# Performance work log

Hardware: AMD Instinct MI355X
Metric: run time of the kernel (lower is better)

The kernel has to match this reference:

```python
import jax, jax.numpy as jnp
import numpy as np

EPS = 1e-05


def setup_inputs() -> dict:
    key = jax.random.key(0)
    kx, kw, kb, kg, kp, kq = jax.random.split(key, 6)
    B, S, D = 32, 1024, 1024
    x = jax.random.normal(kx, (B, S, D), dtype=jnp.float32)
    # Linear(input_size, input_size) params
    W = jax.random.normal(kw, (D, D), dtype=jnp.float32) / np.sqrt(D)
    b = jax.random.normal(kb, (D,), dtype=jnp.float32) * 0.01
    gold_opinion = jax.random.uniform(kg, (B, S, 5), dtype=jnp.float32)
    predict_opinion = jax.random.uniform(kp, (B, S, 5), dtype=jnp.float32)
    gold_prob = jax.random.uniform(kq, (), dtype=jnp.float32)
    return {"x": x, "W": W, "b": b, "gold_opinion": gold_opinion,
            "predict_opinion": predict_opinion, "gold_prob": gold_prob}


def reference(x, W, b, gold_opinion, predict_opinion, gold_prob):
    # x: [B, S, D]
    S = x.shape[-2]
    x_tran = jnp.einsum('bsd,ed->bse', x, W) + b           # Linear: x @ W^T + b
    weights = jnp.einsum('bsd,btd->bst', x_tran, x)        # QK^T -> [B, S, S]

    idx = jnp.arange(S)
    location = jnp.abs(idx[None, :] - idx[:, None]).astype(x.dtype)  # [S, S]
    weights = weights * (1.0 / (location + EPS))           # distance decay

    # use_opinion = True branch
    gold_op = gold_opinion[:, :, 1] + gold_opinion[:, :, 2]          # [B, S]
    pred_op = predict_opinion[:, :, 3] + predict_opinion[:, :, 4]    # [B, S]
    opinion_weights = gold_prob * gold_op + (1.0 - gold_prob) * pred_op
    weights = weights * opinion_weights[:, :, None]

    weights = jnp.exp(jnp.tanh(weights))                   # pseudo-softmax numerator
    off_diag = (location != 0).astype(weights.dtype)       # eye(S) == 0 mask
    weights = weights * off_diag
    weights = weights / (jnp.sum(weights, axis=-1, keepdims=True) + EPS)
    return jnp.einsum('bst,btd->bsd', weights, x)
```

## Files before the change

kernel.cpp:

```cpp
#include <hip/hip_runtime.h>

#define EPSF 1e-5f

typedef _Float16 f16x8 __attribute__((ext_vector_type(8)));
typedef float f32x4 __attribute__((ext_vector_type(4)));

__device__ __forceinline__ void gload_lds16(const _Float16* g, _Float16* l) {
  __builtin_amdgcn_global_load_lds(
      (const __attribute__((address_space(1))) unsigned int*)g,
      (__attribute__((address_space(3))) unsigned int*)l, 16, 0, 0);
}

__device__ __forceinline__ f16x8 cvt8(float4 a, float4 b) {
  f16x8 h;
  h[0] = (_Float16)a.x; h[1] = (_Float16)a.y; h[2] = (_Float16)a.z; h[3] = (_Float16)a.w;
  h[4] = (_Float16)b.x; h[5] = (_Float16)b.y; h[6] = (_Float16)b.z; h[7] = (_Float16)b.w;
  return h;
}

__device__ __forceinline__ float frcp(float x) {
  float r;
  asm("v_rcp_f32 %0, %1" : "=v"(r) : "v"(x));
  return r;
}

__device__ __forceinline__ void gemm256_run(const _Float16* __restrict__ Ag,
                                            const _Float16* __restrict__ Bg,
                                            _Float16* lds, f32x4 (&acc)[8][4]) {
  const int tid = threadIdx.x;
  const int wave = tid >> 6, lane = tid & 63;
  const int wm = wave >> 2, wn = wave & 3;
  const int quad = lane >> 4, nl = lane & 15;
  const int swz = nl & 7;
  const long stg_off = (long)(wave * 8 + (lane >> 3)) * 1024 +
                       (((lane & 7) ^ (lane >> 3)) * 8);

#pragma unroll
  for (int i = 0; i < 8; ++i)
#pragma unroll
    for (int j = 0; j < 4; ++j) acc[i][j] = (f32x4){0.f, 0.f, 0.f, 0.f};

  f16x8 af[4], bf[4];

#define STG(G, T1, q, isB)                                                   \
  gload_lds16((G) + (long)(q) * 65536 + stg_off + (T1) * 64,                 \
              lds + (((T1) & 1) * 32768 + (isB) * 16384 + (q) * 4096 + wave * 512))
#define LDB4(bb, ksub)                                                       \
  {                                                                          \
    const _Float16* pB_ = lds + (bb) * 32768 + 16384 + (wn * 64 + nl) * 64 + \
                          ((((ksub) * 4 + quad) ^ swz) * 8);                 \
    _Pragma("unroll") for (int j_ = 0; j_ < 4; ++j_)                         \
        bf[j_] = *(const f16x8*)(pB_ + j_ * 1024);                           \
  }
#define LDA4(bb, mq, ksub)                                                   \
  {                                                                          \
    const _Float16* pA_ = lds + (bb) * 32768 +                               \
                          (wm * 128 + (mq) * 64 + nl) * 64 +                 \
                          ((((ksub) * 4 + quad) ^ swz) * 8);                 \
    _Pragma("unroll") for (int i_ = 0; i_ < 4; ++i_)                         \
        af[i_] = *(const f16x8*)(pA_ + i_ * 1024);                           \
  }
#define MFMA16(mq)                                                           \
  {                                                                          \
    __builtin_amdgcn_s_setprio(1);                                           \
    _Pragma("unroll") for (int i_ = 0; i_ < 4; ++i_)                         \
        _Pragma("unroll") for (int j_ = 0; j_ < 4; ++j_)                     \
            acc[(mq) * 4 + i_][j_] = __builtin_amdgcn_mfma_f32_16x16x32_f16( \
                af[i_], bf[j_], acc[(mq) * 4 + i_][j_], 0, 0, 0);            \
    __builtin_amdgcn_s_setprio(0);                                           \
  }
#define BAR __builtin_amdgcn_s_barrier()
#define SCHED0 __builtin_amdgcn_sched_barrier(0)
#define LGKM0 asm volatile("s_waitcnt lgkmcnt(0)" ::: "memory")
#define VMW2 asm volatile("s_waitcnt vmcnt(2)" ::: "memory")
#define VMW0 asm volatile("s_waitcnt vmcnt(0)" ::: "memory")

  STG(Bg, 0, 0, 1); STG(Bg, 0, 1, 1);
  STG(Ag, 0, 0, 0); STG(Ag, 0, 2, 0);
  STG(Bg, 0, 2, 1); STG(Bg, 0, 3, 1);
  STG(Ag, 0, 1, 0); STG(Ag, 0, 3, 0);
  VMW2;
  BAR;

#pragma unroll 2
  for (int T = 0; T < 15; ++T) {
    const int bb = T & 1;
    LDB4(bb, 0); LDA4(bb, 0, 0);
    STG(Bg, T + 1, 0, 1); STG(Bg, T + 1, 1, 1);
    SCHED0; BAR; LGKM0; SCHED0; MFMA16(0); VMW2; BAR;
    LDA4(bb, 1, 0);
    STG(Ag, T + 1, 0, 0); STG(Ag, T + 1, 2, 0);
    SCHED0; BAR; LGKM0; SCHED0; MFMA16(1); BAR;
    LDB4(bb, 1); LDA4(bb, 0, 1);
    STG(Bg, T + 1, 2, 1); STG(Bg, T + 1, 3, 1);
    SCHED0; BAR; LGKM0; SCHED0; MFMA16(0); BAR;
    LDA4(bb, 1, 1);
    STG(Ag, T + 1, 1, 0); STG(Ag, T + 1, 3, 0);
    SCHED0; BAR; LGKM0; SCHED0; MFMA16(1); VMW2; BAR;
  }
  {
    LDB4(1, 0); LDA4(1, 0, 0);
    SCHED0; BAR; LGKM0; SCHED0; MFMA16(0); VMW0; BAR;
    LDA4(1, 1, 0);
    SCHED0; BAR; LGKM0; SCHED0; MFMA16(1); BAR;
    LDB4(1, 1); LDA4(1, 0, 1);
    SCHED0; BAR; LGKM0; SCHED0; MFMA16(0); BAR;
    LDA4(1, 1, 1);
    SCHED0; BAR; LGKM0; SCHED0; MFMA16(1); BAR;
  }
#undef VMW0
#undef VMW2
#undef LGKM0
#undef SCHED0
#undef BAR
#undef MFMA16
#undef LDA4
#undef LDB4
#undef STG
}

__global__ void prep_opin_k(const float* __restrict__ gold, const float* __restrict__ pred,
                            const float* __restrict__ gprob, float* __restrict__ opin, int n) {
  int i = blockIdx.x * 256 + threadIdx.x;
  if (i >= n) return;
  float gp = gprob[0];
  float go = gold[i * 5 + 1] + gold[i * 5 + 2];
  float po = pred[i * 5 + 3] + pred[i * 5 + 4];
  opin[i] = gp * go + (1.0f - gp) * po;
}

__global__ __launch_bounds__(256) void prep_h_k(const float* __restrict__ src,
                                                _Float16* __restrict__ dst) {
  long i = ((long)blockIdx.x * 256 + threadIdx.x) * 8;
  float4 a = *(const float4*)(src + i);
  float4 b = *(const float4*)(src + i + 4);
  *(f16x8*)(dst + i) = cvt8(a, b);
}

__global__ __launch_bounds__(256) void prep_x_k(const float* __restrict__ x,
                                                _Float16* __restrict__ Xh,
                                                _Float16* __restrict__ XhT) {
  __shared__ _Float16 T[64][66];
  const int d0 = blockIdx.x * 64, t0 = blockIdx.y * 64;
  const long base = (long)blockIdx.z * 1024;
  const int c = threadIdx.x & 63, tr = threadIdx.x >> 6;
#pragma unroll
  for (int k = 0; k < 16; ++k) {
    int t = k * 4 + tr;
    float v = x[(base + t0 + t) * 1024 + d0 + c];
    _Float16 h = (_Float16)v;
    Xh[(base + t0 + t) * 1024 + d0 + c] = h;
    T[t][c] = h;
  }
  __syncthreads();
#pragma unroll
  for (int k = 0; k < 16; ++k) {
    int d = k * 4 + tr;
    XhT[(base + d0 + d) * 1024 + t0 + c] = T[c][d];
  }
}

__global__ __launch_bounds__(512, 2) void gemm12_k(const _Float16* __restrict__ Xh,
                                                   const _Float16* __restrict__ Wh,
                                                   const float* __restrict__ bias,
                                                   _Float16* __restrict__ XT) {
  __shared__ _Float16 lds[2 * 32768];
  const int lin = blockIdx.x;
  const int ii = lin >> 3;
  const int mt = (lin & 7) * 16 + (ii >> 2);
  const int nt = ii & 3;
  const long m0 = (long)mt * 256;
  const int n0 = nt * 256;

  f32x4 acc[8][4];
  gemm256_run(Xh + m0 * 1024, Wh + (long)n0 * 1024, lds, acc);

  const int tid = threadIdx.x;
  const int wave = tid >> 6, lane = tid & 63;
  const int wm = wave >> 2, wn = wave & 3;
  const int quad = lane >> 4, nl = lane & 15;
#pragma unroll
  for (int mi = 0; mi < 8; ++mi) {
    long gm = m0 + wm * 128 + mi * 16 + quad * 4;
#pragma unroll
    for (int ni = 0; ni < 4; ++ni) {
      int gn = n0 + wn * 64 + ni * 16 + nl;
      float bv = bias[gn];
#pragma unroll
      for (int r = 0; r < 4; ++r)
        XT[(gm + r) * 1024 + gn] = (_Float16)(acc[mi][ni][r] + bv);
    }
  }
}

__global__ __launch_bounds__(512, 2) void scores2_k(const _Float16* __restrict__ XT,
                                                    const _Float16* __restrict__ Xh,
                                                    const float* __restrict__ gold,
                                                    const float* __restrict__ pred,
                                                    const float* __restrict__ gprob,
                                                    _Float16* __restrict__ P,
                                                    float* __restrict__ dpart) {
  __shared__ _Float16 lds[2 * 32768];
  const int lin = blockIdx.x;
  const int ii = lin >> 3;
  const int b = (lin & 7) + 8 * (ii >> 4);
  const int tile = ii & 15;
  const int s0 = (tile >> 2) * 256;
  const int t0 = (tile & 3) * 256;
  const long base = (long)b * 1024;

  f32x4 acc[8][4];
  gemm256_run(XT + (base + s0) * 1024, Xh + (base + t0) * 1024, lds, acc);

  const int tid = threadIdx.x;
  float* sop = (float*)lds;
  if (tid < 256) {
    int s = s0 + tid;
    float gp = gprob[0];
    long o = (base + s) * 5;
    float go = gold[o + 1] + gold[o + 2];
    float po = pred[o + 3] + pred[o + 4];
    sop[tid] = gp * go + (1.0f - gp) * po;
  }
  __syncthreads();

  const int wave = tid >> 6, lane = tid & 63;
  const int wm = wave >> 2, wn = wave & 3;
  const int quad = lane >> 4, nl = lane & 15;
  const int slice = (tile & 3) * 4 + wn;
#pragma unroll
  for (int mi = 0; mi < 8; ++mi) {
#pragma unroll
    for (int r = 0; r < 4; ++r) {
      int sl = wm * 128 + mi * 16 + quad * 4 + r;
      int s = s0 + sl;
      float opv = sop[sl];
      float rs = 0.f;
#pragma unroll
      for (int ni = 0; ni < 4; ++ni) {
        int tc = t0 + wn * 64 + ni * 16 + nl;
        float loc = fabsf((float)(s - tc));
        float arg = acc[mi][ni][r] * frcp(loc + EPSF) * opv;
        float th = 1.f - 2.f * frcp(__expf(2.f * arg) + 1.f);
        float p = __expf(th);
        if (s == tc) p = 0.f;
        P[(base + s) * 1024 + tc] = (_Float16)p;
        rs += p;
      }
      rs += __shfl_xor(rs, 1);
      rs += __shfl_xor(rs, 2);
      rs += __shfl_xor(rs, 4);
      rs += __shfl_xor(rs, 8);
      if (nl == 0) dpart[(((long)slice * 32 + b) << 10) + s] = rs;
    }
  }
}

__global__ __launch_bounds__(512, 2) void pv2_k(const _Float16* __restrict__ P,
                                                const _Float16* __restrict__ XhT,
                                                const float* __restrict__ dpart,
                                                float* __restrict__ out) {
  __shared__ _Float16 lds[2 * 32768];
  const int lin = blockIdx.x;
  const int ii = lin >> 3;
  const int b = (lin & 7) + 8 * (ii >> 4);
  const int tile = ii & 15;
  const int s0 = (tile >> 2) * 256;
  const int d0 = (tile & 3) * 256;
  const long base = (long)b * 1024;

  f32x4 acc[8][4];
  gemm256_run(P + (base + s0) * 1024, XhT + (base + d0) * 1024, lds, acc);

  const int tid = threadIdx.x;
  float* sden = (float*)lds;
  if (tid < 256) {
    float sum = 0.f;
#pragma unroll
    for (int k = 0; k < 16; ++k)
      sum += dpart[(((long)k * 32 + b) << 10) + s0 + tid];
    sden[tid] = frcp(sum + EPSF);
  }
  __syncthreads();

  const int wave = tid >> 6, lane = tid & 63;
  const int wm = wave >> 2, wn = wave & 3;
  const int quad = lane >> 4, nl = lane & 15;
#pragma unroll
  for (int mi = 0; mi < 8; ++mi) {
#pragma unroll
    for (int r = 0; r < 4; ++r) {
      int sl = wm * 128 + mi * 16 + quad * 4 + r;
      int s = s0 + sl;
      float inv = sden[sl];
#pragma unroll
      for (int ni = 0; ni < 4; ++ni) {
        int d = d0 + wn * 64 + ni * 16 + nl;
        out[(base + s) * 1024 + d] = acc[mi][ni][r] * inv;
      }
    }
  }
}

__global__ __launch_bounds__(256) void gemm1_k(const _Float16* __restrict__ Xh,
                                               const float* __restrict__ Wt,
                                               const float* __restrict__ bias,
                                               _Float16* __restrict__ XT) {
  __shared__ _Float16 As[128 * 32];
  __shared__ _Float16 Bs[128 * 32];
  const int tid = threadIdx.x;
  const int wave = tid >> 6, lane = tid & 63;
  const int wm = wave >> 1, wn = wave & 1;
  const int quad = lane >> 4, nl = lane & 15;
  const long m0 = (long)blockIdx.y * 128;
  const int n0 = blockIdx.x * 128;

  f32x4 acc[4][4];
  f32x4 zero = {0.f, 0.f, 0.f, 0.f};
#pragma unroll
  for (int i = 0; i < 4; ++i)
#pragma unroll
    for (int j = 0; j < 4; ++j) acc[i][j] = zero;

  const int crow = tid >> 2;
  const int ckc = (tid & 3) * 8;

  for (int k0 = 0; k0 < 1024; k0 += 32) {
#pragma unroll
    for (int it = 0; it < 2; ++it) {
      int c = it * 256 + tid;
      gload_lds16(Xh + (m0 + (c >> 2)) * 1024 + k0 + (c & 3) * 8,
                  &As[(it * 256 + wave * 64) * 8]);
      int row = it * 64 + crow;
      const float* sb = Wt + (long)(n0 + row) * 1024 + k0 + ckc;
      float4 b0 = *(const float4*)sb;
      float4 b1 = *(const float4*)(sb + 4);
      *(f16x8*)&Bs[row * 32 + ckc] = cvt8(b0, b1);
    }
    __syncthreads();
    f16x8 af[4], bf[4];
#pragma unroll
    for (int mi = 0; mi < 4; ++mi)
      af[mi] = *(const f16x8*)&As[(wm * 64 + mi * 16 + nl) * 32 + quad * 8];
#pragma unroll
    for (int ni = 0; ni < 4; ++ni)
      bf[ni] = *(const f16x8*)&Bs[(wn * 64 + ni * 16 + nl) * 32 + quad * 8];
#pragma unroll
    for (int mi = 0; mi < 4; ++mi)
#pragma unroll
      for (int ni = 0; ni < 4; ++ni)
        acc[mi][ni] = __builtin_amdgcn_mfma_f32_16x16x32_f16(af[mi], bf[ni], acc[mi][ni], 0, 0, 0);
    __syncthreads();
  }

#pragma unroll
  for (int mi = 0; mi < 4; ++mi) {
    long gm = m0 + wm * 64 + mi * 16 + quad * 4;
#pragma unroll
    for (int ni = 0; ni < 4; ++ni) {
      int gn = n0 + wn * 64 + ni * 16 + nl;
      float bv = bias[gn];
#pragma unroll
      for (int r = 0; r < 4; ++r)
        XT[(gm + r) * 1024 + gn] = (_Float16)(acc[mi][ni][r] + bv);
    }
  }
}

__global__ __launch_bounds__(256) void scores_f_k(const _Float16* __restrict__ XT,
                                                  const _Float16* __restrict__ Xh,
                                                  const float* __restrict__ opin,
                                                  _Float16* __restrict__ P,
                                                  float* __restrict__ denom) {
  __shared__ _Float16 As[128 * 32];
  __shared__ _Float16 Bs[128 * 32];
  const int tid = threadIdx.x;
  const int wave = tid >> 6, lane = tid & 63;
  const int wm = wave >> 1, wn = wave & 1;
  const int quad = lane >> 4, nl = lane & 15;
  const int b = blockIdx.z;
  const int s0 = blockIdx.y * 128;
  const int t0 = blockIdx.x * 128;
  const long base = (long)b * 1024;

  f32x4 acc[4][4];
  f32x4 zero = {0.f, 0.f, 0.f, 0.f};
#pragma unroll
  for (int i = 0; i < 4; ++i)
#pragma unroll
    for (int j = 0; j < 4; ++j) acc[i][j] = zero;

  for (int k0 = 0; k0 < 1024; k0 += 32) {
#pragma unroll
    for (int it = 0; it < 2; ++it) {
      int c = it * 256 + tid;
      gload_lds16(XT + (base + s0 + (c >> 2)) * 1024 + k0 + (c & 3) * 8,
                  &As[(it * 256 + wave * 64) * 8]);
      gload_lds16(Xh + (base + t0 + (c >> 2)) * 1024 + k0 + (c & 3) * 8,
                  &Bs[(it * 256 + wave * 64) * 8]);
    }
    __syncthreads();
    f16x8 af[4], bf[4];
#pragma unroll
    for (int mi = 0; mi < 4; ++mi)
      af[mi] = *(const f16x8*)&As[(wm * 64 + mi * 16 + nl) * 32 + quad * 8];
#pragma unroll
    for (int ni = 0; ni < 4; ++ni)
      bf[ni] = *(const f16x8*)&Bs[(wn * 64 + ni * 16 + nl) * 32 + quad * 8];
#pragma unroll
    for (int mi = 0; mi < 4; ++mi)
#pragma unroll
      for (int ni = 0; ni < 4; ++ni)
        acc[mi][ni] = __builtin_amdgcn_mfma_f32_16x16x32_f16(af[mi], bf[ni], acc[mi][ni], 0, 0, 0);
    __syncthreads();
  }

#pragma unroll
  for (int mi = 0; mi < 4; ++mi) {
#pragma unroll
    for (int r = 0; r < 4; ++r) {
      int s = s0 + wm * 64 + mi * 16 + quad * 4 + r;
      float opv = opin[b * 1024 + s];
      float rs = 0.f;
#pragma unroll
      for (int ni = 0; ni < 4; ++ni) {
        int t = t0 + wn * 64 + ni * 16 + nl;
        float loc = fabsf((float)(s - t));
        float arg = acc[mi][ni][r] * (1.0f / (loc + EPSF)) * opv;
        float th = 1.f - 2.f / (__expf(2.f * arg) + 1.f);
        float p = __expf(th);
        if (s == t) p = 0.f;
        P[(base + s) * 1024 + t] = (_Float16)p;
        rs += p;
      }
      rs += __shfl_xor(rs, 1);
      rs += __shfl_xor(rs, 2);
      rs += __shfl_xor(rs, 4);
      rs += __shfl_xor(rs, 8);
      if (nl == 0) atomicAdd(&denom[b * 1024 + s], rs);
    }
  }
}

__global__ __launch_bounds__(256) void pv_k(const _Float16* __restrict__ P,
                                            const float* __restrict__ X,
                                            const float* __restrict__ denom,
                                            float* __restrict__ out) {
  __shared__ _Float16 As[128 * 32];
  __shared__ _Float16 BsT[128 * 40];
  const int tid = threadIdx.x;
  const int wave = tid >> 6, lane = tid & 63;
  const int wm = wave >> 1, wn = wave & 1;
  const int quad = lane >> 4, nl = lane & 15;
  const int b = blockIdx.z;
  const int s0 = blockIdx.y * 128;
  const int d0 = blockIdx.x * 128;
  const long base = (long)b * 1024;

  const int dcol = tid & 127;
  const int tg = tid >> 7;

  f32x4 acc[4][4];
  f32x4 zero = {0.f, 0.f, 0.f, 0.f};
#pragma unroll
  for (int i = 0; i < 4; ++i)
#pragma unroll
    for (int j = 0; j < 4; ++j) acc[i][j] = zero;

  for (int k0 = 0; k0 < 1024; k0 += 32) {
#pragma unroll
    for (int it = 0; it < 2; ++it) {
      int c = it * 256 + tid;
      gload_lds16(P + (base + s0 + (c >> 2)) * 1024 + k0 + (c & 3) * 8,
                  &As[(it * 256 + wave * 64) * 8]);
    }
    {
      const float* xb = X + (base + k0 + tg * 16) * 1024 + d0 + dcol;
      float v[16];
#pragma unroll
      for (int j = 0; j < 16; ++j) v[j] = xb[j * 1024];
      f16x8 h0, h1;
#pragma unroll
      for (int j = 0; j < 8; ++j) { h0[j] = (_Float16)v[j]; h1[j] = (_Float16)v[8 + j]; }
      *(f16x8*)&BsT[dcol * 40 + tg * 16] = h0;
      *(f16x8*)&BsT[dcol * 40 + tg * 16 + 8] = h1;
    }
    __syncthreads();
    f16x8 af[4], bf[4];
#pragma unroll
    for (int mi = 0; mi < 4; ++mi)
      af[mi] = *(const f16x8*)&As[(wm * 64 + mi * 16 + nl) * 32 + quad * 8];
#pragma unroll
    for (int ni = 0; ni < 4; ++ni)
      bf[ni] = *(const f16x8*)&BsT[(wn * 64 + ni * 16 + nl) * 40 + quad * 8];
#pragma unroll
    for (int mi = 0; mi < 4; ++mi)
#pragma unroll
      for (int ni = 0; ni < 4; ++ni)
        acc[mi][ni] = __builtin_amdgcn_mfma_f32_16x16x32_f16(af[mi], bf[ni], acc[mi][ni], 0, 0, 0);
    __syncthreads();
  }

#pragma unroll
  for (int mi = 0; mi < 4; ++mi) {
#pragma unroll
    for (int r = 0; r < 4; ++r) {
      int s = s0 + wm * 64 + mi * 16 + quad * 4 + r;
      float inv = 1.0f / (denom[b * 1024 + s] + EPSF);
#pragma unroll
      for (int ni = 0; ni < 4; ++ni) {
        int d = d0 + wn * 64 + ni * 16 + nl;
        out[(base + s) * 1024 + d] = acc[mi][ni][r] * inv;
      }
    }
  }
}

extern "C" void kernel_launch(void* const* d_in, const int* in_sizes, int n_in,
                              void* d_out, int out_size, void* d_ws, size_t ws_size,
                              hipStream_t stream) {
  (void)in_sizes; (void)n_in; (void)out_size;
  const int B = 32, S = 1024;
  const int BS = B * S;

  const float* x     = (const float*)d_in[0];
  const float* W     = (const float*)d_in[1];
  const float* bias  = (const float*)d_in[2];
  const float* gold  = (const float*)d_in[3];
  const float* pred  = (const float*)d_in[4];
  const float* gprob = (const float*)d_in[5];

  const size_t P_BYTES  = (size_t)BS * 1024 * sizeof(_Float16);
  const size_t XT_BYTES = P_BYTES;
  const size_t DP_B     = (size_t)16 * BS * sizeof(float);
  const size_t WH_B     = (size_t)1024 * 1024 * sizeof(_Float16);
  const size_t OPIN_B   = (size_t)BS * sizeof(float);
  const size_t NEED_BIG = P_BYTES + XT_BYTES + DP_B + WH_B;

  char* ws = (char*)d_ws;
  _Float16* P = (_Float16*)ws;
  const bool big = ws_size >= NEED_BIG;

  _Float16* XT = (_Float16*)d_out;
  _Float16* Xh = XT + (size_t)BS * 1024;
  float* out   = (float*)d_out;

  if (big) {
    _Float16* XhT = (_Float16*)(ws + P_BYTES);
    float* dpart  = (float*)(ws + P_BYTES + XT_BYTES);
    _Float16* Wh  = (_Float16*)(ws + P_BYTES + XT_BYTES + DP_B);

    prep_x_k<<<dim3(16, 16, 32), 256, 0, stream>>>(x, Xh, XhT);
    prep_h_k<<<(1024 * 1024 / 8) / 256, 256, 0, stream>>>(W, Wh);
    gemm12_k<<<512, 512, 0, stream>>>(Xh, Wh, bias, XT);
    scores2_k<<<512, 512, 0, stream>>>(XT, Xh, gold, pred, gprob, P, dpart);
    pv2_k<<<512, 512, 0, stream>>>(P, XhT, dpart, out);
  } else {
    float* opin  = (float*)(ws + P_BYTES);
    float* denom = opin + BS;

    hipMemsetAsync(denom, 0, OPIN_B, stream);
    prep_opin_k<<<BS / 256, 256, 0, stream>>>(gold, pred, gprob, opin, BS);
    prep_h_k<<<(BS * 1024 / 8) / 256, 256, 0, stream>>>(x, Xh);
    gemm1_k<<<dim3(8, 256), 256, 0, stream>>>(Xh, W, bias, XT);
    scores_f_k<<<dim3(8, 8, 32), 256, 0, stream>>>(XT, Xh, opin, P, denom);
    pv_k<<<dim3(8, 8, 32), 256, 0, stream>>>(P, x, denom, out);
  }
}
```

Measured before the change: 489.5 us.

## Restructure shared GEMM mainloop to 4-stage pipeline with 32-wide K tiles

The shared 256x256 GEMM core changes from a double-buffered K=64 tile loop to a quadruple-buffered K=32 tile loop that prefetches three tiles ahead. The staging addressing, swizzle and LDS read offsets are rewritten to match the narrower tile, and the vmcnt waits are adjusted to the deeper pipeline. The aim is to hide global-to-LDS load latency better in all three GEMM kernels while keeping the same total LDS size. The cost is twice as many barriers per unit of K and the risk that the new swizzle adds LDS bank conflicts.

```diff
diff --git a/kernel.cpp b/kernel.cpp
--- a/kernel.cpp
+++ b/kernel.cpp
@@ -31,9 +31,8 @@
   const int wave = tid >> 6, lane = tid & 63;
   const int wm = wave >> 2, wn = wave & 3;
   const int quad = lane >> 4, nl = lane & 15;
-  const int swz = nl & 7;
-  const long stg_off = (long)(wave * 8 + (lane >> 3)) * 1024 +
-                       (((lane & 7) ^ (lane >> 3)) * 8);
+  const int swz = (nl >> 1) & 3;
+  const long stg_off = (long)(tid >> 2) * 1024 + (((tid & 3) ^ ((tid >> 3) & 3)) * 8);
 
 #pragma unroll
   for (int i = 0; i < 8; ++i)
@@ -42,23 +41,22 @@
 
   f16x8 af[4], bf[4];
 
-#define STG(G, T1, q, isB)                                                   \
-  gload_lds16((G) + (long)(q) * 65536 + stg_off + (T1) * 64,                 \
-              lds + (((T1) & 1) * 32768 + (isB) * 16384 + (q) * 4096 + wave * 512))
-#define LDB4(bb, ksub)                                                       \
+#define STG(G, Tidx, h, isB, SBUF)                                           \
+  gload_lds16((G) + (long)(h) * 131072 + stg_off + (Tidx) * 32,              \
+              lds + (SBUF) * 16384 + (isB) * 8192 + (h) * 4096 + wave * 512)
+#define LDB4(BUF)                                                            \
   {                                                                          \
-    const _Float16* pB_ = lds + (bb) * 32768 + 16384 + (wn * 64 + nl) * 64 + \
-                          ((((ksub) * 4 + quad) ^ swz) * 8);                 \
+    const _Float16* pB_ = lds + (BUF) * 16384 + 8192 +                       \
+                          (wn * 64 + nl) * 32 + ((quad ^ swz) * 8);          \
     _Pragma("unroll") for (int j_ = 0; j_ < 4; ++j_)                         \
-        bf[j_] = *(const f16x8*)(pB_ + j_ * 1024);                           \
-  }
-#define LDA4(bb, mq, ksub)                                                   \
+        bf[j_] = *(const f16x8*)(pB_ + j_ * 512);                            \
+  }
+#define LDA4(BUF, mq)                                                        \
   {                                                                          \
-    const _Float16* pA_ = lds + (bb) * 32768 +                               \
-                          (wm * 128 + (mq) * 64 + nl) * 64 +                 \
-                          ((((ksub) * 4 + quad) ^ swz) * 8);                 \
+    const _Float16* pA_ = lds + (BUF) * 16384 +                              \
+                          (wm * 128 + (mq) * 64 + nl) * 32 + ((quad ^ swz) * 8); \
     _Pragma("unroll") for (int i_ = 0; i_ < 4; ++i_)                         \
-        af[i_] = *(const f16x8*)(pA_ + i_ * 1024);                           \
+        af[i_] = *(const f16x8*)(pA_ + i_ * 512);                            \
   }
 #define MFMA16(mq)                                                           \
   {                                                                          \
@@ -72,44 +70,42 @@
 #define BAR __builtin_amdgcn_s_barrier()
 #define SCHED0 __builtin_amdgcn_sched_barrier(0)
 #define LGKM0 asm volatile("s_waitcnt lgkmcnt(0)" ::: "memory")
-#define VMW2 asm volatile("s_waitcnt vmcnt(2)" ::: "memory")
+#define VMW8 asm volatile("s_waitcnt vmcnt(8)" ::: "memory")
+#define VMW4 asm volatile("s_waitcnt vmcnt(4)" ::: "memory")
 #define VMW0 asm volatile("s_waitcnt vmcnt(0)" ::: "memory")
-
-  STG(Bg, 0, 0, 1); STG(Bg, 0, 1, 1);
-  STG(Ag, 0, 0, 0); STG(Ag, 0, 2, 0);
-  STG(Bg, 0, 2, 1); STG(Bg, 0, 3, 1);
-  STG(Ag, 0, 1, 0); STG(Ag, 0, 3, 0);
-  VMW2;
+#define VMNONE
+#define TILE(T, BUF, SBUF, DOSTG, VW)                                        \
+  {                                                                          \
+    LDB4(BUF); LDA4(BUF, 0);                                                 \
+    if (DOSTG) { STG(Bg, (T) + 3, 0, 1, SBUF); STG(Bg, (T) + 3, 1, 1, SBUF); } \
+    SCHED0; BAR; LGKM0; SCHED0; MFMA16(0); BAR;                              \
+    LDA4(BUF, 1);                                                            \
+    if (DOSTG) { STG(Ag, (T) + 3, 0, 0, SBUF); STG(Ag, (T) + 3, 1, 0, SBUF); } \
+    SCHED0; BAR; LGKM0; SCHED0; MFMA16(1); VW; BAR;                          \
+  }
+
+  STG(Bg, 0, 0, 1, 0); STG(Bg, 0, 1, 1, 0); STG(Ag, 0, 0, 0, 0); STG(Ag, 0, 1, 0, 0);
+  STG(Bg, 1, 0, 1, 1); STG(Bg, 1, 1, 1, 1); STG(Ag, 1, 0, 0, 1); STG(Ag, 1, 1, 0, 1);
+  STG(Bg, 2, 0, 1, 2); STG(Bg, 2, 1, 1, 2); STG(Ag, 2, 0, 0, 2); STG(Ag, 2, 1, 0, 2);
+  VMW8;
   BAR;
 
-#pragma unroll 2
-  for (int T = 0; T < 15; ++T) {
-    const int bb = T & 1;
-    LDB4(bb, 0); LDA4(bb, 0, 0);
-    STG(Bg, T + 1, 0, 1); STG(Bg, T + 1, 1, 1);
-    SCHED0; BAR; LGKM0; SCHED0; MFMA16(0); VMW2; BAR;
-    LDA4(bb, 1, 0);
-    STG(Ag, T + 1, 0, 0); STG(Ag, T + 1, 2, 0);
-    SCHED0; BAR; LGKM0; SCHED0; MFMA16(1); BAR;
-    LDB4(bb, 1); LDA4(bb, 0, 1);
-    STG(Bg, T + 1, 2, 1); STG(Bg, T + 1, 3, 1);
-    SCHED0; BAR; LGKM0; SCHED0; MFMA16(0); BAR;
-    LDA4(bb, 1, 1);
-    STG(Ag, T + 1, 1, 0); STG(Ag, T + 1, 3, 0);
-    SCHED0; BAR; LGKM0; SCHED0; MFMA16(1); VMW2; BAR;
-  }
-  {
-    LDB4(1, 0); LDA4(1, 0, 0);
-    SCHED0; BAR; LGKM0; SCHED0; MFMA16(0); VMW0; BAR;
-    LDA4(1, 1, 0);
-    SCHED0; BAR; LGKM0; SCHED0; MFMA16(1); BAR;
-    LDB4(1, 1); LDA4(1, 0, 1);
-    SCHED0; BAR; LGKM0; SCHED0; MFMA16(0); BAR;
-    LDA4(1, 1, 1);
-    SCHED0; BAR; LGKM0; SCHED0; MFMA16(1); BAR;
-  }
+  for (int TT = 0; TT < 28; TT += 4) {
+    TILE(TT + 0, 0, 3, true, VMW8);
+    TILE(TT + 1, 1, 0, true, VMW8);
+    TILE(TT + 2, 2, 1, true, VMW8);
+    TILE(TT + 3, 3, 2, true, VMW8);
+  }
+  TILE(28, 0, 3, true, VMW8);
+  TILE(29, 1, 0, false, VMW4);
+  TILE(30, 2, 0, false, VMW0);
+  TILE(31, 3, 0, false, VMNONE);
+
+#undef TILE
+#undef VMNONE
 #undef VMW0
-#undef VMW2
+#undef VMW4
+#undef VMW8
 #undef LGKM0
 #undef SCHED0
 #undef BAR
@@ -164,7 +160,7 @@
                                                    const _Float16* __restrict__ Wh,
                                                    const float* __restrict__ bias,
                                                    _Float16* __restrict__ XT) {
-  __shared__ _Float16 lds[2 * 32768];
+  __shared__ _Float16 lds[4 * 16384];
   const int lin = blockIdx.x;
   const int ii = lin >> 3;
   const int mt = (lin & 7) * 16 + (ii >> 2);
@@ -200,7 +196,7 @@
                                                     const float* __restrict__ gprob,
                                                     _Float16* __restrict__ P,
                                                     float* __restrict__ dpart) {
-  __shared__ _Float16 lds[2 * 32768];
+  __shared__ _Float16 lds[4 * 16384];
   const int lin = blockIdx.x;
   const int ii = lin >> 3;
   const int b = (lin & 7) + 8 * (ii >> 4);
@@ -260,7 +256,7 @@
                                                 const _Float16* __restrict__ XhT,
                                                 const float* __restrict__ dpart,
                                                 float* __restrict__ out) {
-  __shared__ _Float16 lds[2 * 32768];
+  __shared__ _Float16 lds[4 * 16384];
   const int lin = blockIdx.x;
   const int ii = lin >> 3;
   const int b = (lin & 7) + 8 * (ii >> 4);
```

Result: no change. 480.9 us (-1.7%).
